# Optimization experiments

Hardware: AMD Instinct MI355X
Metric: run time of the kernel (lower is better)

Reference implementation:

```python
import jax, jax.numpy as jnp
import numpy as np

B, CIN, COUT, N, H, W = 8, 64, 64, 16, 32, 32

def cell_centered_grid(h, w):
    # (h, w, h, w, 4) cell-centered coords in [0,1], then mapped to [-1,1]
    dims = (h, w, h, w)
    axes = [(jnp.arange(d, dtype=jnp.float32) + 0.5) / d for d in dims]
    mesh = jnp.meshgrid(*axes, indexing='ij')
    coords = jnp.stack(mesh, axis=-1)
    return 2.0 * coords - 1.0

def setup_inputs() -> dict:
    key = jax.random.key(0)
    ks = jax.random.split(key, 9)
    v = jax.random.normal(ks[0], (B, CIN, H, W), dtype=jnp.float32)
    params = jax.random.normal(ks[1], (N, COUT, CIN), dtype=jnp.float32) / np.sqrt(N * CIN)
    # coeff_mlp: Linear(4,8) -> GELU -> Linear(8,N), torch default init
    w1 = jax.random.uniform(ks[2], (8, 4), jnp.float32, -1/np.sqrt(4), 1/np.sqrt(4))
    b1 = jax.random.uniform(ks[3], (8,), jnp.float32, -1/np.sqrt(4), 1/np.sqrt(4))
    w2 = jax.random.uniform(ks[4], (N, 8), jnp.float32, -1/np.sqrt(8), 1/np.sqrt(8))
    b2 = jax.random.uniform(ks[5], (N,), jnp.float32, -1/np.sqrt(8), 1/np.sqrt(8))
    # 1x1 conv
    cstd = 1/np.sqrt(CIN)
    conv_w = jax.random.uniform(ks[6], (COUT, CIN), jnp.float32, -cstd, cstd)
    conv_b = jax.random.uniform(ks[7], (COUT,), jnp.float32, -cstd, cstd)
    bias = jax.random.uniform(ks[8], (COUT, 1, 1), jnp.float32, -cstd, cstd)
    return {"v": v, "params": params, "w1": w1, "b1": b1, "w2": w2, "b2": b2,
            "conv_w": conv_w, "conv_b": conv_b, "bias": bias}

def reference(v, params, w1, b1, w2, b2, conv_w, conv_b, bias):
    h, w = v.shape[-2], v.shape[-1]
    coords = cell_centered_grid(h, w)                       # (h1,w1,h2,w2,4)
    hid = jax.nn.gelu(coords @ w1.T + b1, approximate=False)
    coeffs = hid @ w2.T + b2                                # (h1,w1,h2,w2,n)
    # contract coeffs with v over input spatial dims first (small intermediate)
    tmp = jnp.einsum('xyhwn,bixy->bnihw', coeffs, v)        # (B,n,i,h2,w2)
    t = jnp.einsum('bnihw,noi->bohw', tmp, params) / (h * w)
    conv = jnp.einsum('bihw,oi->bohw', v, conv_w) + conv_b[None, :, None, None]
    out = t + conv + bias[None]
    return out
```

## Files before the change

### kernel.cpp

```cpp
#include <hip/hip_runtime.h>
#include <hip/hip_bf16.h>
#include <math.h>

#define WSB_LTAB  0u
#define WSB_QM    262144u
#define WSB_RB2   393216u
#define WSB_WPART 409600u
#define WSB_VSUMP 2506752u

#define COS8_INIT {0.98078528f, 0.83146961f, 0.55557023f, 0.19509032f, \
                  -0.19509032f, -0.55557023f, -0.83146961f, -0.98078528f}

__device__ inline float gelu_exact(float z) {
    return 0.5f * z * (1.0f + erff(z * 0.70710678118f));
}

__device__ inline float cheb_hwid(const float* w1, int c) {
    return fmaxf((fabsf(w1[c * 4 + 2]) + fabsf(w1[c * 4 + 3])) * (31.0f / 32.0f), 1e-2f);
}

__global__ __launch_bounds__(256) void wgemm_kernel(const float* __restrict__ v,
                                                    const float* __restrict__ params,
                                                    const float* __restrict__ w1,
                                                    const float* __restrict__ b1,
                                                    const float* __restrict__ w2,
                                                    const float* __restrict__ b2,
                                                    char* __restrict__ wsb) {
    const float COS8[8] = COS8_INIT;
    float* Ltab  = (float*)(wsb + WSB_LTAB);
    float* Qm    = (float*)(wsb + WSB_QM);
    float* Rb2   = (float*)(wsb + WSB_RB2);
    float* Wpart = (float*)(wsb + WSB_WPART);
    float* VsumP = (float*)(wsb + WSB_VSUMP);
    __shared__ float Vs[16][68];
    __shared__ float Gs[64][64];
    int t = threadIdx.x;
    int bi0 = blockIdx.x * 16, xy0 = blockIdx.y * 64;
    {
        int r = t >> 4, c4 = t & 15;
        *(float4*)&Vs[r][c4 * 4] = *(const float4*)(v + (bi0 + r) * 1024 + xy0 + c4 * 4);
    }
    #pragma unroll
    for (int l = 0; l < 16; l++) {
        int e = t + l * 256;
        int xyl = e >> 6, cr = e & 63, c = cr >> 3, r = cr & 7;
        int xy = xy0 + xyl;
        float cx = 2.0f * (((xy >> 5) + 0.5f) / 32.0f) - 1.0f;
        float cy = 2.0f * (((xy & 31) + 0.5f) / 32.0f) - 1.0f;
        float z = cx * w1[c * 4 + 0] + cy * w1[c * 4 + 1] + b1[c]
                + cheb_hwid(w1, c) * COS8[r];
        Gs[xyl][cr] = gelu_exact(z);
    }
    __syncthreads();
    int bl = t >> 4, crq = t & 15;
    float4 acc = make_float4(0.f, 0.f, 0.f, 0.f);
    float vs = 0.0f;
    #pragma unroll 8
    for (int xy = 0; xy < 64; xy++) {
        float a = Vs[bl][xy];
        float4 g = *(const float4*)&Gs[xy][crq * 4];
        acc.x += a * g.x; acc.y += a * g.y; acc.z += a * g.z; acc.w += a * g.w;
        vs += a;
    }
    *(float4*)(Wpart + (size_t)blockIdx.y * 32768 + (bi0 + bl) * 64 + crq * 4) = acc;
    if (crq == 0) VsumP[blockIdx.y * 512 + bi0 + bl] = vs;

    int bid = blockIdx.y * 32 + blockIdx.x;
    int u = bid * 200 + t;
    if (t < 200) {
        if (u < 65536) {
            int cr = u >> 10, hw = u & 1023, c = cr >> 3, r = cr & 7;
            float hwid = cheb_hwid(w1, c);
            float ch = 2.0f * (((hw >> 5) + 0.5f) / 32.0f) - 1.0f;
            float cw = 2.0f * (((hw & 31) + 0.5f) / 32.0f) - 1.0f;
            float vv = ch * w1[c * 4 + 2] + cw * w1[c * 4 + 3];
            float tr = hwid * COS8[r];
            float p = 1.0f, d = 1.0f;
            #pragma unroll
            for (int s = 0; s < 8; s++)
                if (s != r) {
                    float ts = hwid * COS8[s];
                    p *= (vv - ts);
                    d *= (tr - ts);
                }
            Ltab[u] = p / d;
        } else if (u < 98304) {
            int u2 = u - 65536;
            int c = u2 >> 12, oi = u2 & 4095;
            float s = 0.0f;
            #pragma unroll
            for (int n = 0; n < 16; n++)
                s += params[n * 4096 + oi] * w2[n * 8 + c];
            Qm[u2] = s * (1.0f / 1024.0f);
        } else {
            int oi = u - 98304;
            float s = 0.0f;
            #pragma unroll
            for (int n = 0; n < 16; n++)
                s += params[n * 4096 + oi] * b2[n];
            Rb2[oi] = s * (1.0f / 1024.0f);
        }
    }
}

__global__ __launch_bounds__(512) void final_kernel(const float* __restrict__ v,
                                                    const float* __restrict__ conv_w,
                                                    const float* __restrict__ conv_b,
                                                    const float* __restrict__ bias,
                                                    float* __restrict__ out,
                                                    char* __restrict__ wsb) {
    const float* Ltab  = (const float*)(wsb + WSB_LTAB);
    const float* Qm    = (const float*)(wsb + WSB_QM);
    const float* Rb2   = (const float*)(wsb + WSB_RB2);
    const float* Wpart = (const float*)(wsb + WSB_WPART);
    const float* VsumP = (const float*)(wsb + WSB_VSUMP);
    __shared__ float Ct[128 * 36];
    __shared__ float Ys[128 * 64];
    __shared__ float Ws[64 * 64];
    __shared__ float Esh[32];
    __shared__ float Vsh[64];
    int t = threadIdx.x;
    int hw0 = blockIdx.x * 64, o0 = blockIdx.y * 32, b = blockIdx.z;

    {
        int e0 = t * 8;
        float4 a0 = make_float4(0.f, 0.f, 0.f, 0.f);
        float4 a1 = make_float4(0.f, 0.f, 0.f, 0.f);
        const float* wp = Wpart + b * 4096 + e0;
        #pragma unroll
        for (int ks = 0; ks < 16; ks++) {
            const float4* p = (const float4*)(wp + (size_t)ks * 32768);
            float4 x0 = p[0], x1 = p[1];
            a0.x += x0.x; a0.y += x0.y; a0.z += x0.z; a0.w += x0.w;
            a1.x += x1.x; a1.y += x1.y; a1.z += x1.z; a1.w += x1.w;
        }
        *(float4*)&Ws[e0]     = a0;
        *(float4*)&Ws[e0 + 4] = a1;
    }
    if (t < 64) {
        float s = 0.0f;
        #pragma unroll
        for (int ks = 0; ks < 16; ks++) s += VsumP[ks * 512 + b * 64 + t];
        Vsh[t] = s;
    }
    #pragma unroll
    for (int l = 0; l < 4; l++) {
        int e = t + l * 512;
        int kk = e >> 5, ol = e & 31;
        Ct[(64 + kk) * 36 + ol] = conv_w[(o0 + ol) * 64 + kk];
    }
    #pragma unroll
    for (int l = 0; l < 2; l++) {
        int f = t + l * 512;
        int k = f >> 4, q = f & 15;
        *(float4*)&Ys[(64 + k) * 64 + q * 4] =
            *(const float4*)(v + (size_t)b * 65536 + k * 1024 + hw0 + q * 4);
    }
    #pragma unroll
    for (int l = 0; l < 2; l++) {
        int f = t + l * 512;
        int k = f >> 4, q = f & 15;
        *(float4*)&Ys[k * 64 + q * 4] =
            *(const float4*)(Ltab + (size_t)k * 1024 + hw0 + q * 4);
    }
    __syncthreads();

    {
        int ol = t >> 4, c = (t >> 1) & 7, hi = t & 1;
        float a[4] = {};
        const float* qrow = Qm + c * 4096 + (o0 + ol) * 64;
        for (int i = 0; i < 64; i++) {
            float q = qrow[i];
            float4 w = *(const float4*)&Ws[i * 64 + c * 8 + hi * 4];
            a[0] += q * w.x; a[1] += q * w.y; a[2] += q * w.z; a[3] += q * w.w;
        }
        #pragma unroll
        for (int j = 0; j < 4; j++)
            Ct[(c * 8 + hi * 4 + j) * 36 + ol] = a[j];
    }
    if (t < 32) {
        int o = o0 + t;
        float s = conv_b[o] + bias[o];
        const float* rr = Rb2 + o * 64;
        for (int i = 0; i < 64; i++) s += rr[i] * Vsh[i];
        Esh[t] = s;
    }
    __syncthreads();

    int g = t >> 8, tt = t & 255;
    int ty = tt >> 5, tx = tt & 31;
    float acc[4][2];
    #pragma unroll
    for (int m = 0; m < 4; m++) {
        float e = (g == 0) ? Esh[ty * 4 + m] : 0.0f;
        acc[m][0] = e; acc[m][1] = e;
    }
    #pragma unroll 4
    for (int k = 0; k < 64; k++) {
        int kk = g * 64 + k;
        float4 cq = *(const float4*)&Ct[kk * 36 + ty * 4];
        float2 y = *(const float2*)&Ys[kk * 64 + tx * 2];
        acc[0][0] += cq.x * y.x; acc[0][1] += cq.x * y.y;
        acc[1][0] += cq.y * y.x; acc[1][1] += cq.y * y.y;
        acc[2][0] += cq.z * y.x; acc[2][1] += cq.z * y.y;
        acc[3][0] += cq.w * y.x; acc[3][1] += cq.w * y.y;
    }
    if (g == 1) {
        *(float4*)&Ws[tt * 8]     = make_float4(acc[0][0], acc[0][1], acc[1][0], acc[1][1]);
        *(float4*)&Ws[tt * 8 + 4] = make_float4(acc[2][0], acc[2][1], acc[3][0], acc[3][1]);
    }
    __syncthreads();
    if (g == 0) {
        float4 p0 = *(const float4*)&Ws[tt * 8];
        float4 p1 = *(const float4*)&Ws[tt * 8 + 4];
        acc[0][0] += p0.x; acc[0][1] += p0.y; acc[1][0] += p0.z; acc[1][1] += p0.w;
        acc[2][0] += p1.x; acc[2][1] += p1.y; acc[3][0] += p1.z; acc[3][1] += p1.w;
        #pragma unroll
        for (int m = 0; m < 4; m++) {
            *(float2*)(out + (size_t)b * 65536 + (o0 + ty * 4 + m) * 1024 + hw0 + tx * 2)
                = make_float2(acc[m][0], acc[m][1]);
        }
    }
}

extern "C" void kernel_launch(void* const* d_in, const int* in_sizes, int n_in,
                              void* d_out, int out_size, void* d_ws, size_t ws_size,
                              hipStream_t stream) {
    const float* v      = (const float*)d_in[0];
    const float* params = (const float*)d_in[1];
    const float* w1     = (const float*)d_in[2];
    const float* b1     = (const float*)d_in[3];
    const float* w2     = (const float*)d_in[4];
    const float* b2     = (const float*)d_in[5];
    const float* conv_w = (const float*)d_in[6];
    const float* conv_b = (const float*)d_in[7];
    const float* bias   = (const float*)d_in[8];
    float* out = (float*)d_out;
    char* wsb  = (char*)d_ws;

    wgemm_kernel<<<dim3(32, 16), 256, 0, stream>>>(v, params, w1, b1, w2, b2, wsb);
    final_kernel<<<dim3(16, 2, 8), 512, 0, stream>>>(v, conv_w, conv_b, bias, out, wsb);
}
```

Baseline: 88.57 us.

## Fuse two kernels into one persistent kernel with a software grid barrier

```diff
diff --git a/kernel.cpp b/kernel.cpp
--- a/kernel.cpp
+++ b/kernel.cpp
@@ -1,5 +1,4 @@
 #include <hip/hip_runtime.h>
-#include <hip/hip_bf16.h>
 #include <math.h>
 
 #define WSB_LTAB  0u
@@ -19,206 +18,231 @@
     return fmaxf((fabsf(w1[c * 4 + 2]) + fabsf(w1[c * 4 + 3])) * (31.0f / 32.0f), 1e-2f);
 }
 
-__global__ __launch_bounds__(256) void wgemm_kernel(const float* __restrict__ v,
-                                                    const float* __restrict__ params,
-                                                    const float* __restrict__ w1,
-                                                    const float* __restrict__ b1,
-                                                    const float* __restrict__ w2,
-                                                    const float* __restrict__ b2,
-                                                    char* __restrict__ wsb) {
+__device__ unsigned int g_count = 0;
+__device__ unsigned int g_gen = 0;
+
+__device__ inline void grid_sync_n(unsigned int nblocks) {
+    __syncthreads();
+    if (threadIdx.x == 0) {
+        __threadfence();
+        unsigned int gen = __hip_atomic_load(&g_gen, __ATOMIC_ACQUIRE,
+                                             __HIP_MEMORY_SCOPE_AGENT);
+        unsigned int arrived = __hip_atomic_fetch_add(&g_count, 1u, __ATOMIC_ACQ_REL,
+                                                      __HIP_MEMORY_SCOPE_AGENT) + 1u;
+        if (arrived == nblocks) {
+            __hip_atomic_store(&g_count, 0u, __ATOMIC_RELAXED,
+                               __HIP_MEMORY_SCOPE_AGENT);
+            __hip_atomic_fetch_add(&g_gen, 1u, __ATOMIC_RELEASE,
+                                   __HIP_MEMORY_SCOPE_AGENT);
+        } else {
+            while (__hip_atomic_load(&g_gen, __ATOMIC_ACQUIRE,
+                                     __HIP_MEMORY_SCOPE_AGENT) == gen)
+                __builtin_amdgcn_s_sleep(2);
+        }
+        __threadfence();
+    }
+    __syncthreads();
+}
+
+__global__ __launch_bounds__(512, 2) void fused_kernel(
+        const float* __restrict__ v,      const float* __restrict__ params,
+        const float* __restrict__ w1,     const float* __restrict__ b1,
+        const float* __restrict__ w2,     const float* __restrict__ b2,
+        const float* __restrict__ conv_w, const float* __restrict__ conv_b,
+        const float* __restrict__ bias,   float* __restrict__ out,
+        char* __restrict__ wsb) {
     const float COS8[8] = COS8_INIT;
     float* Ltab  = (float*)(wsb + WSB_LTAB);
     float* Qm    = (float*)(wsb + WSB_QM);
     float* Rb2   = (float*)(wsb + WSB_RB2);
     float* Wpart = (float*)(wsb + WSB_WPART);
     float* VsumP = (float*)(wsb + WSB_VSUMP);
-    __shared__ float Vs[16][68];
-    __shared__ float Gs[64][64];
+    __shared__ float smem[16992];
     int t = threadIdx.x;
-    int bi0 = blockIdx.x * 16, xy0 = blockIdx.y * 64;
+
     {
-        int r = t >> 4, c4 = t & 15;
-        *(float4*)&Vs[r][c4 * 4] = *(const float4*)(v + (bi0 + r) * 1024 + xy0 + c4 * 4);
+        int h = t >> 8, tl = t & 255;
+        int orig = blockIdx.x * 2 + h;
+        int bx = orig & 31, by = orig >> 5;
+        float* Vs = smem + h * 5184;
+        float* Gs = smem + h * 5184 + 1088;
+        int bi0 = bx * 16, xy0 = by * 64;
+        {
+            int r = tl >> 4, c4 = tl & 15;
+            *(float4*)&Vs[r * 68 + c4 * 4] =
+                *(const float4*)(v + (bi0 + r) * 1024 + xy0 + c4 * 4);
+        }
+        #pragma unroll
+        for (int l = 0; l < 16; l++) {
+            int e = tl + l * 256;
+            int xyl = e >> 6, cr = e & 63, c = cr >> 3, r = cr & 7;
+            int xy = xy0 + xyl;
+            float cx = 2.0f * (((xy >> 5) + 0.5f) / 32.0f) - 1.0f;
+            float cy = 2.0f * (((xy & 31) + 0.5f) / 32.0f) - 1.0f;
+            float z = cx * w1[c * 4 + 0] + cy * w1[c * 4 + 1] + b1[c]
+                    + cheb_hwid(w1, c) * COS8[r];
+            Gs[xyl * 64 + cr] = gelu_exact(z);
+        }
+        __syncthreads();
+        int bl = tl >> 4, crq = tl & 15;
+        float4 acc = make_float4(0.f, 0.f, 0.f, 0.f);
+        float vs = 0.0f;
+        #pragma unroll 8
+        for (int xy = 0; xy < 64; xy++) {
+            float a = Vs[bl * 68 + xy];
+            float4 g = *(const float4*)&Gs[xy * 64 + crq * 4];
+            acc.x += a * g.x; acc.y += a * g.y; acc.z += a * g.z; acc.w += a * g.w;
+            vs += a;
+        }
+        *(float4*)(Wpart + (size_t)by * 32768 + (bi0 + bl) * 64 + crq * 4) = acc;
+        if (crq == 0) VsumP[by * 512 + bi0 + bl] = vs;
+
+        int u = (by * 32 + bx) * 200 + tl;
+        if (tl < 200) {
+            if (u < 65536) {
+                int cr = u >> 10, hw = u & 1023, c = cr >> 3, r = cr & 7;
+                float hwid = cheb_hwid(w1, c);
+                float ch = 2.0f * (((hw >> 5) + 0.5f) / 32.0f) - 1.0f;
+                float cw = 2.0f * (((hw & 31) + 0.5f) / 32.0f) - 1.0f;
+                float vv = ch * w1[c * 4 + 2] + cw * w1[c * 4 + 3];
+                float tr = hwid * COS8[r];
+                float p = 1.0f, d = 1.0f;
+                #pragma unroll
+                for (int s = 0; s < 8; s++)
+                    if (s != r) {
+                        float ts = hwid * COS8[s];
+                        p *= (vv - ts);
+                        d *= (tr - ts);
+                    }
+                Ltab[u] = p / d;
+            } else if (u < 98304) {
+                int u2 = u - 65536;
+                int c = u2 >> 12, oi = u2 & 4095;
+                float s = 0.0f;
+                #pragma unroll
+                for (int n = 0; n < 16; n++)
+                    s += params[n * 4096 + oi] * w2[n * 8 + c];
+                Qm[u2] = s * (1.0f / 1024.0f);
+            } else {
+                int oi = u - 98304;
+                float s = 0.0f;
+                #pragma unroll
+                for (int n = 0; n < 16; n++)
+                    s += params[n * 4096 + oi] * b2[n];
+                Rb2[oi] = s * (1.0f / 1024.0f);
+            }
+        }
     }
-    #pragma unroll
-    for (int l = 0; l < 16; l++) {
-        int e = t + l * 256;
-        int xyl = e >> 6, cr = e & 63, c = cr >> 3, r = cr & 7;
-        int xy = xy0 + xyl;
-        float cx = 2.0f * (((xy >> 5) + 0.5f) / 32.0f) - 1.0f;
-        float cy = 2.0f * (((xy & 31) + 0.5f) / 32.0f) - 1.0f;
-        float z = cx * w1[c * 4 + 0] + cy * w1[c * 4 + 1] + b1[c]
-                + cheb_hwid(w1, c) * COS8[r];
-        Gs[xyl][cr] = gelu_exact(z);
-    }
-    __syncthreads();
-    int bl = t >> 4, crq = t & 15;
-    float4 acc = make_float4(0.f, 0.f, 0.f, 0.f);
-    float vs = 0.0f;
-    #pragma unroll 8
-    for (int xy = 0; xy < 64; xy++) {
-        float a = Vs[bl][xy];
-        float4 g = *(const float4*)&Gs[xy][crq * 4];
-        acc.x += a * g.x; acc.y += a * g.y; acc.z += a * g.z; acc.w += a * g.w;
-        vs += a;
-    }
-    *(float4*)(Wpart + (size_t)blockIdx.y * 32768 + (bi0 + bl) * 64 + crq * 4) = acc;
-    if (crq == 0) VsumP[blockIdx.y * 512 + bi0 + bl] = vs;
-
-    int bid = blockIdx.y * 32 + blockIdx.x;
-    int u = bid * 200 + t;
-    if (t < 200) {
-        if (u < 65536) {
-            int cr = u >> 10, hw = u & 1023, c = cr >> 3, r = cr & 7;
-            float hwid = cheb_hwid(w1, c);
-            float ch = 2.0f * (((hw >> 5) + 0.5f) / 32.0f) - 1.0f;
-            float cw = 2.0f * (((hw & 31) + 0.5f) / 32.0f) - 1.0f;
-            float vv = ch * w1[c * 4 + 2] + cw * w1[c * 4 + 3];
-            float tr = hwid * COS8[r];
-            float p = 1.0f, d = 1.0f;
-            #pragma unroll
-            for (int s = 0; s < 8; s++)
-                if (s != r) {
-                    float ts = hwid * COS8[s];
-                    p *= (vv - ts);
-                    d *= (tr - ts);
-                }
-            Ltab[u] = p / d;
-        } else if (u < 98304) {
-            int u2 = u - 65536;
-            int c = u2 >> 12, oi = u2 & 4095;
+
+    grid_sync_n(256u);
+
+    {
+        float* Ct  = smem;
+        float* Ys  = smem + 4608;
+        float* Ws  = smem + 12800;
+        float* Esh = smem + 16896;
+        float* Vsh = smem + 16928;
+        int bf = blockIdx.x;
+        int hw0 = (bf & 15) * 64, o0 = ((bf >> 4) & 1) * 32, b = bf >> 5;
+
+        {
+            int e0 = t * 8;
+            float4 a0 = make_float4(0.f, 0.f, 0.f, 0.f);
+            float4 a1 = make_float4(0.f, 0.f, 0.f, 0.f);
+            const float* wp = Wpart + b * 4096 + e0;
+            #pragma unroll
+            for (int ks = 0; ks < 16; ks++) {
+                const float4* p = (const float4*)(wp + (size_t)ks * 32768);
+                float4 x0 = p[0], x1 = p[1];
+                a0.x += x0.x; a0.y += x0.y; a0.z += x0.z; a0.w += x0.w;
+                a1.x += x1.x; a1.y += x1.y; a1.z += x1.z; a1.w += x1.w;
+            }
+            *(float4*)&Ws[e0]     = a0;
+            *(float4*)&Ws[e0 + 4] = a1;
+        }
+        if (t < 64) {
             float s = 0.0f;
             #pragma unroll
-            for (int n = 0; n < 16; n++)
-                s += params[n * 4096 + oi] * w2[n * 8 + c];
-            Qm[u2] = s * (1.0f / 1024.0f);
-        } else {
-            int oi = u - 98304;
-            float s = 0.0f;
-            #pragma unroll
-            for (int n = 0; n < 16; n++)
-                s += params[n * 4096 + oi] * b2[n];
-            Rb2[oi] = s * (1.0f / 1024.0f);
-        }
-    }
-}
-
-__global__ __launch_bounds__(512) void final_kernel(const float* __restrict__ v,
-                                                    const float* __restrict__ conv_w,
-                                                    const float* __restrict__ conv_b,
-                                                    const float* __restrict__ bias,
-                                                    float* __restrict__ out,
-                                                    char* __restrict__ wsb) {
-    const float* Ltab  = (const float*)(wsb + WSB_LTAB);
-    const float* Qm    = (const float*)(wsb + WSB_QM);
-    const float* Rb2   = (const float*)(wsb + WSB_RB2);
-    const float* Wpart = (const float*)(wsb + WSB_WPART);
-    const float* VsumP = (const float*)(wsb + WSB_VSUMP);
-    __shared__ float Ct[128 * 36];
-    __shared__ float Ys[128 * 64];
-    __shared__ float Ws[64 * 64];
-    __shared__ float Esh[32];
-    __shared__ float Vsh[64];
-    int t = threadIdx.x;
-    int hw0 = blockIdx.x * 64, o0 = blockIdx.y * 32, b = blockIdx.z;
-
-    {
-        int e0 = t * 8;
-        float4 a0 = make_float4(0.f, 0.f, 0.f, 0.f);
-        float4 a1 = make_float4(0.f, 0.f, 0.f, 0.f);
-        const float* wp = Wpart + b * 4096 + e0;
-        #pragma unroll
-        for (int ks = 0; ks < 16; ks++) {
-            const float4* p = (const float4*)(wp + (size_t)ks * 32768);
-            float4 x0 = p[0], x1 = p[1];
-            a0.x += x0.x; a0.y += x0.y; a0.z += x0.z; a0.w += x0.w;
-            a1.x += x1.x; a1.y += x1.y; a1.z += x1.z; a1.w += x1.w;
-        }
-        *(float4*)&Ws[e0]     = a0;
-        *(float4*)&Ws[e0 + 4] = a1;
-    }
-    if (t < 64) {
-        float s = 0.0f;
-        #pragma unroll
-        for (int ks = 0; ks < 16; ks++) s += VsumP[ks * 512 + b * 64 + t];
-        Vsh[t] = s;
-    }
-    #pragma unroll
-    for (int l = 0; l < 4; l++) {
-        int e = t + l * 512;
-        int kk = e >> 5, ol = e & 31;
-        Ct[(64 + kk) * 36 + ol] = conv_w[(o0 + ol) * 64 + kk];
-    }
-    #pragma unroll
-    for (int l = 0; l < 2; l++) {
-        int f = t + l * 512;
-        int k = f >> 4, q = f & 15;
-        *(float4*)&Ys[(64 + k) * 64 + q * 4] =
-            *(const float4*)(v + (size_t)b * 65536 + k * 1024 + hw0 + q * 4);
-    }
-    #pragma unroll
-    for (int l = 0; l < 2; l++) {
-        int f = t + l * 512;
-        int k = f >> 4, q = f & 15;
-        *(float4*)&Ys[k * 64 + q * 4] =
-            *(const float4*)(Ltab + (size_t)k * 1024 + hw0 + q * 4);
-    }
-    __syncthreads();
-
-    {
-        int ol = t >> 4, c = (t >> 1) & 7, hi = t & 1;
-        float a[4] = {};
-        const float* qrow = Qm + c * 4096 + (o0 + ol) * 64;
-        for (int i = 0; i < 64; i++) {
-            float q = qrow[i];
-            float4 w = *(const float4*)&Ws[i * 64 + c * 8 + hi * 4];
-            a[0] += q * w.x; a[1] += q * w.y; a[2] += q * w.z; a[3] += q * w.w;
-        }
-        #pragma unroll
-        for (int j = 0; j < 4; j++)
-            Ct[(c * 8 + hi * 4 + j) * 36 + ol] = a[j];
-    }
-    if (t < 32) {
-        int o = o0 + t;
-        float s = conv_b[o] + bias[o];
-        const float* rr = Rb2 + o * 64;
-        for (int i = 0; i < 64; i++) s += rr[i] * Vsh[i];
-        Esh[t] = s;
-    }
-    __syncthreads();
-
-    int g = t >> 8, tt = t & 255;
-    int ty = tt >> 5, tx = tt & 31;
-    float acc[4][2];
-    #pragma unroll
-    for (int m = 0; m < 4; m++) {
-        float e = (g == 0) ? Esh[ty * 4 + m] : 0.0f;
-        acc[m][0] = e; acc[m][1] = e;
-    }
-    #pragma unroll 4
-    for (int k = 0; k < 64; k++) {
-        int kk = g * 64 + k;
-        float4 cq = *(const float4*)&Ct[kk * 36 + ty * 4];
-        float2 y = *(const float2*)&Ys[kk * 64 + tx * 2];
-        acc[0][0] += cq.x * y.x; acc[0][1] += cq.x * y.y;
-        acc[1][0] += cq.y * y.x; acc[1][1] += cq.y * y.y;
-        acc[2][0] += cq.z * y.x; acc[2][1] += cq.z * y.y;
-        acc[3][0] += cq.w * y.x; acc[3][1] += cq.w * y.y;
-    }
-    if (g == 1) {
-        *(float4*)&Ws[tt * 8]     = make_float4(acc[0][0], acc[0][1], acc[1][0], acc[1][1]);
-        *(float4*)&Ws[tt * 8 + 4] = make_float4(acc[2][0], acc[2][1], acc[3][0], acc[3][1]);
-    }
-    __syncthreads();
-    if (g == 0) {
-        float4 p0 = *(const float4*)&Ws[tt * 8];
-        float4 p1 = *(const float4*)&Ws[tt * 8 + 4];
-        acc[0][0] += p0.x; acc[0][1] += p0.y; acc[1][0] += p0.z; acc[1][1] += p0.w;
-        acc[2][0] += p1.x; acc[2][1] += p1.y; acc[3][0] += p1.z; acc[3][1] += p1.w;
+            for (int ks = 0; ks < 16; ks++) s += VsumP[ks * 512 + b * 64 + t];
+            Vsh[t] = s;
+        }
+        #pragma unroll
+        for (int l = 0; l < 4; l++) {
+            int e = t + l * 512;
+            int kk = e >> 5, oc = e & 31;
+            Ct[(64 + kk) * 36 + oc] = conv_w[(o0 + oc) * 64 + kk];
+        }
+        #pragma unroll
+        for (int l = 0; l < 2; l++) {
+            int f = t + l * 512;
+            int k = f >> 4, q = f & 15;
+            *(float4*)&Ys[(64 + k) * 64 + q * 4] =
+                *(const float4*)(v + (size_t)b * 65536 + k * 1024 + hw0 + q * 4);
+        }
+        #pragma unroll
+        for (int l = 0; l < 2; l++) {
+            int f = t + l * 512;
+            int k = f >> 4, q = f & 15;
+            *(float4*)&Ys[k * 64 + q * 4] =
+                *(const float4*)(Ltab + (size_t)k * 1024 + hw0 + q * 4);
+        }
+        __syncthreads();
+
+        {
+            int ol = t >> 4, c = (t >> 1) & 7, hi = t & 1;
+            float a[4] = {};
+            const float* qrow = Qm + c * 4096 + (o0 + ol) * 64;
+            for (int i = 0; i < 64; i++) {
+                float q = qrow[i];
+                float4 w = *(const float4*)&Ws[i * 64 + c * 8 + hi * 4];
+                a[0] += q * w.x; a[1] += q * w.y; a[2] += q * w.z; a[3] += q * w.w;
+            }
+            #pragma unroll
+            for (int j = 0; j < 4; j++)
+                Ct[(c * 8 + hi * 4 + j) * 36 + ol] = a[j];
+        }
+        if (t < 32) {
+            int o = o0 + t;
+            float s = conv_b[o] + bias[o];
+            const float* rr = Rb2 + o * 64;
+            for (int i = 0; i < 64; i++) s += rr[i] * Vsh[i];
+            Esh[t] = s;
+        }
+        __syncthreads();
+
+        int g = t >> 8, tt = t & 255;
+        int ty = tt >> 5, tx = tt & 31;
+        float acc[4][2];
         #pragma unroll
         for (int m = 0; m < 4; m++) {
-            *(float2*)(out + (size_t)b * 65536 + (o0 + ty * 4 + m) * 1024 + hw0 + tx * 2)
-                = make_float2(acc[m][0], acc[m][1]);
+            float e = (g == 0) ? Esh[ty * 4 + m] : 0.0f;
+            acc[m][0] = e; acc[m][1] = e;
+        }
+        #pragma unroll 4
+        for (int k = 0; k < 64; k++) {
+            int kk = g * 64 + k;
+            float4 cq = *(const float4*)&Ct[kk * 36 + ty * 4];
+            float2 y = *(const float2*)&Ys[kk * 64 + tx * 2];
+            acc[0][0] += cq.x * y.x; acc[0][1] += cq.x * y.y;
+            acc[1][0] += cq.y * y.x; acc[1][1] += cq.y * y.y;
+            acc[2][0] += cq.z * y.x; acc[2][1] += cq.z * y.y;
+            acc[3][0] += cq.w * y.x; acc[3][1] += cq.w * y.y;
+        }
+        if (g == 1) {
+            *(float4*)&Ws[tt * 8]     = make_float4(acc[0][0], acc[0][1], acc[1][0], acc[1][1]);
+            *(float4*)&Ws[tt * 8 + 4] = make_float4(acc[2][0], acc[2][1], acc[3][0], acc[3][1]);
+        }
+        __syncthreads();
+        if (g == 0) {
+            float4 p0 = *(const float4*)&Ws[tt * 8];
+            float4 p1 = *(const float4*)&Ws[tt * 8 + 4];
+            acc[0][0] += p0.x; acc[0][1] += p0.y; acc[1][0] += p0.z; acc[1][1] += p0.w;
+            acc[2][0] += p1.x; acc[2][1] += p1.y; acc[3][0] += p1.z; acc[3][1] += p1.w;
+            #pragma unroll
+            for (int m = 0; m < 4; m++) {
+                *(float2*)(out + (size_t)b * 65536 + (o0 + ty * 4 + m) * 1024 + hw0 + tx * 2)
+                    = make_float2(acc[m][0], acc[m][1]);
+            }
         }
     }
 }
@@ -238,6 +262,6 @@
     float* out = (float*)d_out;
     char* wsb  = (char*)d_ws;
 
-    wgemm_kernel<<<dim3(32, 16), 256, 0, stream>>>(v, params, w1, b1, w2, b2, wsb);
-    final_kernel<<<dim3(16, 2, 8), 512, 0, stream>>>(v, conv_w, conv_b, bias, out, wsb);
-}
+    fused_kernel<<<dim3(256), 512, 0, stream>>>(v, params, w1, b1, w2, b2,
+                                                conv_w, conv_b, bias, out, wsb);
+}
```

Measured after the change: 121.6 us. +37.3%, slower.
